# Kernel optimization log

Measured on AMD Instinct MI355X. Metric: run time of the kernel, lower is better.

The kernel has to match this reference:

```python
import jax, jax.numpy as jnp
import numpy as np

NUM_NODES = 127   # complete binary tree of depth 7: parent(i) = (i-1)//2
BATCH = 262144
DEPTH = 7


def _project(p):
    """DAG min-propagation in topological order, vectorized per tree level.

    Equivalent to: for parent in topo_order: for child in children(parent):
        p[:, child] = min(p[:, child], p[:, parent])
    Each child has exactly one parent, and parents are always processed before
    children when sweeping levels top-down, so level-parallel updates match the
    edge-sequential reference exactly.
    """
    for level in range(1, DEPTH):
        start, end = 2 ** level - 1, 2 ** (level + 1) - 1
        idx = jnp.arange(start, end)          # children at this level
        par = (idx - 1) // 2                  # their unique parents
        p = p.at[:, idx].set(jnp.minimum(p[:, idx], p[:, par]))
    return p


def setup_inputs() -> dict:
    key = jax.random.key(0)
    x = jax.random.normal(key, (BATCH, NUM_NODES), dtype=jnp.float32)
    return {"x": x}


def reference(x):
    # DAGConstraintLayer.forward: sigmoid then hard DAG projection
    return _project(jax.nn.sigmoid(x))
```

## Files before the change

### kernel.cpp

```cpp
#include <hip/hip_runtime.h>


#define NODES 127
#define RPW   8
#define WPB   4
#define RPB   (RPW * WPB)
#define BLOCK 256
#define WF4   ((RPW * NODES) / 4)

typedef float v4 __attribute__((ext_vector_type(4)));
typedef const __attribute__((address_space(1))) v4* gp4;
typedef __attribute__((address_space(3))) v4* lp4;

__device__ __forceinline__ float sigf(float v) {
    float e = __builtin_amdgcn_exp2f(v * -1.44269504089f);
    return __builtin_amdgcn_rcpf(1.0f + e);
}

__global__ __launch_bounds__(BLOCK) void dag_kernel(const float* __restrict__ x,
                                                    float* __restrict__ out) {
    __shared__ float buf[RPB * NODES];
    v4* b4 = (v4*)buf;

    const int t    = threadIdx.x;
    const int lane = t & 63;
    const int w    = t >> 6;
    const size_t blk = (size_t)blockIdx.x * (RPB * NODES);
    const v4* src4 = (const v4*)(x + blk);
    v4*       dst4 = (v4*)(out + blk);
    const int wf4 = w * WF4;

    #pragma unroll
    for (int k = 0; k < 3; ++k) {
        int idx = wf4 + k * 64 + lane;
        __builtin_amdgcn_global_load_lds((gp4)(src4 + idx), (lp4)(b4 + idx), 16, 0, 0);
    }
    if (lane < 62) {
        int idx = wf4 + 192 + lane;
        __builtin_amdgcn_global_load_lds((gp4)(src4 + idx), (lp4)(b4 + idx), 16, 0, 0);
    }
    __builtin_amdgcn_s_waitcnt(0x0F70);

    const int r = lane >> 3;
    const int s = lane & 7;
    const int o = w * (RPW * NODES) + r * NODES;

    float x0 = buf[o + 0], x1 = buf[o + 1], x2 = buf[o + 2], x3 = buf[o + 3];
    float x4 = buf[o + 4], x5 = buf[o + 5], x6 = buf[o + 6];
    float r3  = buf[o + 7 + s];
    float r40 = buf[o + 15 + 2 * s], r41 = buf[o + 16 + 2 * s];
    float r50 = buf[o + 31 + 4 * s], r51 = buf[o + 32 + 4 * s];
    float r52 = buf[o + 33 + 4 * s], r53 = buf[o + 34 + 4 * s];
    float r60 = buf[o + 63 + 8 * s], r61 = buf[o + 64 + 8 * s];
    float r62 = buf[o + 65 + 8 * s], r63 = buf[o + 66 + 8 * s];
    float r64 = buf[o + 67 + 8 * s], r65 = buf[o + 68 + 8 * s];
    float r66 = buf[o + 69 + 8 * s], r67 = buf[o + 70 + 8 * s];

    float p1 = fminf(x0, x1), p2 = fminf(x0, x2);
    float p3 = fminf(p1, x3), p4 = fminf(p1, x4);
    float p5 = fminf(p2, x5), p6 = fminf(p2, x6);

    float pa = (s & 4) ? ((s & 2) ? p6 : p5) : ((s & 2) ? p4 : p3);

    float v3  = fminf(pa, r3);
    float v40 = fminf(v3, r40),  v41 = fminf(v3, r41);
    float v50 = fminf(v40, r50), v51 = fminf(v40, r51);
    float v52 = fminf(v41, r52), v53 = fminf(v41, r53);
    float v60 = fminf(v50, r60), v61 = fminf(v50, r61);
    float v62 = fminf(v51, r62), v63 = fminf(v51, r63);
    float v64 = fminf(v52, r64), v65 = fminf(v52, r65);
    float v66 = fminf(v53, r66), v67 = fminf(v53, r67);

    buf[o + 7 + s]      = sigf(v3);
    buf[o + 15 + 2 * s] = sigf(v40);  buf[o + 16 + 2 * s] = sigf(v41);
    buf[o + 31 + 4 * s] = sigf(v50);  buf[o + 32 + 4 * s] = sigf(v51);
    buf[o + 33 + 4 * s] = sigf(v52);  buf[o + 34 + 4 * s] = sigf(v53);
    buf[o + 63 + 8 * s] = sigf(v60);  buf[o + 64 + 8 * s] = sigf(v61);
    buf[o + 65 + 8 * s] = sigf(v62);  buf[o + 66 + 8 * s] = sigf(v63);
    buf[o + 67 + 8 * s] = sigf(v64);  buf[o + 68 + 8 * s] = sigf(v65);
    buf[o + 69 + 8 * s] = sigf(v66);  buf[o + 70 + 8 * s] = sigf(v67);

    float ta = (s & 1) ? ((s & 2) ? p3 : p1) : ((s & 2) ? p2 : x0);
    float tb = (s & 1) ? p5 : ((s & 2) ? p6 : p4);
    float vt = (s & 4) ? tb : ta;
    if (s < 7) buf[o + s] = sigf(vt);

    #pragma unroll
    for (int k = 0; k < 3; ++k) {
        int idx = wf4 + k * 64 + lane;
        __builtin_nontemporal_store(b4[idx], dst4 + idx);
    }
    if (lane < 62) {
        int idx = wf4 + 192 + lane;
        __builtin_nontemporal_store(b4[idx], dst4 + idx);
    }
}

extern "C" void kernel_launch(void* const* d_in, const int* in_sizes, int n_in,
                              void* d_out, int out_size, void* d_ws, size_t ws_size,
                              hipStream_t stream) {
    const float* x = (const float*)d_in[0];
    float* out = (float*)d_out;
    int rows = in_sizes[0] / NODES;
    int grid = rows / RPB;
    dag_kernel<<<grid, BLOCK, 0, stream>>>(x, out);
}
```

Measured before the change: 235.7 us.

## Use persistent grid with per-wave double-buffered async loads into LDS

Replaces the one-tile-per-block launch with a fixed grid of 1024 blocks. Each wave loops over 8-row tiles and prefetches the next tile into a second LDS buffer while it computes the current one. The aim is to overlap global load latency with compute and stores, and to avoid the cost of launching many short blocks. The loop assumes the tile count divides evenly by the number of waves, otherwise rows would be dropped. Output stores also change from nontemporal to regular stores, and the doubled LDS use may lower occupancy.

```diff
diff --git a/kernel.cpp b/kernel.cpp
--- a/kernel.cpp
+++ b/kernel.cpp
@@ -4,9 +4,10 @@
 #define NODES 127
 #define RPW   8
 #define WPB   4
-#define RPB   (RPW * WPB)
 #define BLOCK 256
-#define WF4   ((RPW * NODES) / 4)
+#define TPW   (RPW * NODES)
+#define TF4   (TPW / 4)
+#define GRID  1024
 
 typedef float v4 __attribute__((ext_vector_type(4)));
 typedef const __attribute__((address_space(1))) v4* gp4;
@@ -17,82 +18,91 @@
     return __builtin_amdgcn_rcpf(1.0f + e);
 }
 
+__device__ __forceinline__ void issue_loads(const v4* __restrict__ src4, int tf4,
+                                            lp4 ldst, int lane) {
+    #pragma unroll
+    for (int k = 0; k < 3; ++k)
+        __builtin_amdgcn_global_load_lds((gp4)(src4 + tf4 + k * 64 + lane),
+                                         ldst + k * 64 + lane, 16, 0, 0);
+    if (lane < 62)
+        __builtin_amdgcn_global_load_lds((gp4)(src4 + tf4 + 192 + lane),
+                                         ldst + 192 + lane, 16, 0, 0);
+}
+
 __global__ __launch_bounds__(BLOCK) void dag_kernel(const float* __restrict__ x,
-                                                    float* __restrict__ out) {
-    __shared__ float buf[RPB * NODES];
-    v4* b4 = (v4*)buf;
-
+                                                    float* __restrict__ out,
+                                                    int ntiles) {
+    __shared__ float buf[WPB][2][TPW];
     const int t    = threadIdx.x;
     const int lane = t & 63;
     const int w    = t >> 6;
-    const size_t blk = (size_t)blockIdx.x * (RPB * NODES);
-    const v4* src4 = (const v4*)(x + blk);
-    v4*       dst4 = (v4*)(out + blk);
-    const int wf4 = w * WF4;
+    const int wid  = blockIdx.x * WPB + w;
+    const int nw   = GRID * WPB;
+    const int iters = ntiles / nw;
 
-    #pragma unroll
-    for (int k = 0; k < 3; ++k) {
-        int idx = wf4 + k * 64 + lane;
-        __builtin_amdgcn_global_load_lds((gp4)(src4 + idx), (lp4)(b4 + idx), 16, 0, 0);
-    }
-    if (lane < 62) {
-        int idx = wf4 + 192 + lane;
-        __builtin_amdgcn_global_load_lds((gp4)(src4 + idx), (lp4)(b4 + idx), 16, 0, 0);
-    }
-    __builtin_amdgcn_s_waitcnt(0x0F70);
-
+    const v4* src4 = (const v4*)x;
+    v4*       dst4 = (v4*)out;
     const int r = lane >> 3;
     const int s = lane & 7;
-    const int o = w * (RPW * NODES) + r * NODES;
+    const int o = r * NODES;
 
-    float x0 = buf[o + 0], x1 = buf[o + 1], x2 = buf[o + 2], x3 = buf[o + 3];
-    float x4 = buf[o + 4], x5 = buf[o + 5], x6 = buf[o + 6];
-    float r3  = buf[o + 7 + s];
-    float r40 = buf[o + 15 + 2 * s], r41 = buf[o + 16 + 2 * s];
-    float r50 = buf[o + 31 + 4 * s], r51 = buf[o + 32 + 4 * s];
-    float r52 = buf[o + 33 + 4 * s], r53 = buf[o + 34 + 4 * s];
-    float r60 = buf[o + 63 + 8 * s], r61 = buf[o + 64 + 8 * s];
-    float r62 = buf[o + 65 + 8 * s], r63 = buf[o + 66 + 8 * s];
-    float r64 = buf[o + 67 + 8 * s], r65 = buf[o + 68 + 8 * s];
-    float r66 = buf[o + 69 + 8 * s], r67 = buf[o + 70 + 8 * s];
+    issue_loads(src4, wid * TF4, (lp4)&buf[w][0][0], lane);
 
-    float p1 = fminf(x0, x1), p2 = fminf(x0, x2);
-    float p3 = fminf(p1, x3), p4 = fminf(p1, x4);
-    float p5 = fminf(p2, x5), p6 = fminf(p2, x6);
+    for (int it = 0; it < iters; ++it) {
+        const int cur = it & 1;
+        if (it == 0) __builtin_amdgcn_s_waitcnt(0x0F70);
+        else         __builtin_amdgcn_s_waitcnt(0x0F74);
+        if (it + 1 < iters)
+            issue_loads(src4, (wid + (it + 1) * nw) * TF4, (lp4)&buf[w][cur ^ 1][0], lane);
 
-    float pa = (s & 4) ? ((s & 2) ? p6 : p5) : ((s & 2) ? p4 : p3);
+        float* lb = &buf[w][cur][0];
 
-    float v3  = fminf(pa, r3);
-    float v40 = fminf(v3, r40),  v41 = fminf(v3, r41);
-    float v50 = fminf(v40, r50), v51 = fminf(v40, r51);
-    float v52 = fminf(v41, r52), v53 = fminf(v41, r53);
-    float v60 = fminf(v50, r60), v61 = fminf(v50, r61);
-    float v62 = fminf(v51, r62), v63 = fminf(v51, r63);
-    float v64 = fminf(v52, r64), v65 = fminf(v52, r65);
-    float v66 = fminf(v53, r66), v67 = fminf(v53, r67);
+        float x0 = lb[o + 0], x1 = lb[o + 1], x2 = lb[o + 2], x3 = lb[o + 3];
+        float x4_ = lb[o + 4], x5 = lb[o + 5], x6 = lb[o + 6];
+        float r3  = lb[o + 7 + s];
+        float r40 = lb[o + 15 + 2 * s], r41 = lb[o + 16 + 2 * s];
+        float r50 = lb[o + 31 + 4 * s], r51 = lb[o + 32 + 4 * s];
+        float r52 = lb[o + 33 + 4 * s], r53 = lb[o + 34 + 4 * s];
+        float r60 = lb[o + 63 + 8 * s], r61 = lb[o + 64 + 8 * s];
+        float r62 = lb[o + 65 + 8 * s], r63 = lb[o + 66 + 8 * s];
+        float r64 = lb[o + 67 + 8 * s], r65 = lb[o + 68 + 8 * s];
+        float r66 = lb[o + 69 + 8 * s], r67 = lb[o + 70 + 8 * s];
 
-    buf[o + 7 + s]      = sigf(v3);
-    buf[o + 15 + 2 * s] = sigf(v40);  buf[o + 16 + 2 * s] = sigf(v41);
-    buf[o + 31 + 4 * s] = sigf(v50);  buf[o + 32 + 4 * s] = sigf(v51);
-    buf[o + 33 + 4 * s] = sigf(v52);  buf[o + 34 + 4 * s] = sigf(v53);
-    buf[o + 63 + 8 * s] = sigf(v60);  buf[o + 64 + 8 * s] = sigf(v61);
-    buf[o + 65 + 8 * s] = sigf(v62);  buf[o + 66 + 8 * s] = sigf(v63);
-    buf[o + 67 + 8 * s] = sigf(v64);  buf[o + 68 + 8 * s] = sigf(v65);
-    buf[o + 69 + 8 * s] = sigf(v66);  buf[o + 70 + 8 * s] = sigf(v67);
+        float p1 = fminf(x0, x1), p2 = fminf(x0, x2);
+        float p3 = fminf(p1, x3), p4 = fminf(p1, x4_);
+        float p5 = fminf(p2, x5), p6 = fminf(p2, x6);
+        float pa = (s & 4) ? ((s & 2) ? p6 : p5) : ((s & 2) ? p4 : p3);
 
-    float ta = (s & 1) ? ((s & 2) ? p3 : p1) : ((s & 2) ? p2 : x0);
-    float tb = (s & 1) ? p5 : ((s & 2) ? p6 : p4);
-    float vt = (s & 4) ? tb : ta;
-    if (s < 7) buf[o + s] = sigf(vt);
+        float v3  = fminf(pa, r3);
+        float v40 = fminf(v3, r40),  v41 = fminf(v3, r41);
+        float v50 = fminf(v40, r50), v51 = fminf(v40, r51);
+        float v52 = fminf(v41, r52), v53 = fminf(v41, r53);
+        float v60 = fminf(v50, r60), v61 = fminf(v50, r61);
+        float v62 = fminf(v51, r62), v63 = fminf(v51, r63);
+        float v64 = fminf(v52, r64), v65 = fminf(v52, r65);
+        float v66 = fminf(v53, r66), v67 = fminf(v53, r67);
 
-    #pragma unroll
-    for (int k = 0; k < 3; ++k) {
-        int idx = wf4 + k * 64 + lane;
-        __builtin_nontemporal_store(b4[idx], dst4 + idx);
-    }
-    if (lane < 62) {
-        int idx = wf4 + 192 + lane;
-        __builtin_nontemporal_store(b4[idx], dst4 + idx);
+        lb[o + 7 + s]      = sigf(v3);
+        lb[o + 15 + 2 * s] = sigf(v40);  lb[o + 16 + 2 * s] = sigf(v41);
+        lb[o + 31 + 4 * s] = sigf(v50);  lb[o + 32 + 4 * s] = sigf(v51);
+        lb[o + 33 + 4 * s] = sigf(v52);  lb[o + 34 + 4 * s] = sigf(v53);
+        lb[o + 63 + 8 * s] = sigf(v60);  lb[o + 64 + 8 * s] = sigf(v61);
+        lb[o + 65 + 8 * s] = sigf(v62);  lb[o + 66 + 8 * s] = sigf(v63);
+        lb[o + 67 + 8 * s] = sigf(v64);  lb[o + 68 + 8 * s] = sigf(v65);
+        lb[o + 69 + 8 * s] = sigf(v66);  lb[o + 70 + 8 * s] = sigf(v67);
+
+        float ta = (s & 1) ? ((s & 2) ? p3 : p1) : ((s & 2) ? p2 : x0);
+        float tb = (s & 1) ? p5 : ((s & 2) ? p6 : p4);
+        float vt = (s & 4) ? tb : ta;
+        if (s < 7) lb[o + s] = sigf(vt);
+
+        const int tb4 = (wid + it * nw) * TF4;
+        v4* lb4 = (v4*)lb;
+        #pragma unroll
+        for (int k = 0; k < 3; ++k)
+            dst4[tb4 + k * 64 + lane] = lb4[k * 64 + lane];
+        if (lane < 62)
+            dst4[tb4 + 192 + lane] = lb4[192 + lane];
     }
 }
 
@@ -101,7 +111,7 @@
                               hipStream_t stream) {
     const float* x = (const float*)d_in[0];
     float* out = (float*)d_out;
-    int rows = in_sizes[0] / NODES;
-    int grid = rows / RPB;
-    dag_kernel<<<grid, BLOCK, 0, stream>>>(x, out);
+    int rows   = in_sizes[0] / NODES;
+    int ntiles = rows / RPW;
+    dag_kernel<<<GRID, BLOCK, 0, stream>>>(x, out, ntiles);
 }
```

New measurement: 230.8 us. -2.1%, faster.
